# Optimization experiments

Measured on AMD Instinct MI355X. Metric: run time of the kernel, lower is better.

Reference implementation:

```python
import jax, jax.numpy as jnp
import numpy as np

C0, C1 = 16, 16
V, E = 100000, 1600000
TWO_PI = 6.2831853


def setup_inputs() -> dict:
    key = jax.random.key(0)
    ks = jax.random.split(key, 12)
    s0 = 1.0 / np.sqrt(C0)
    s1 = 1.0 / np.sqrt(C1)
    return {
        "x": jax.random.normal(ks[0], (V, C0 + 2 * C1), dtype=jnp.float32),
        "edge_index": jax.random.randint(ks[1], (2, E), 0, V, dtype=jnp.int64),
        "angles": jax.random.uniform(ks[2], (E,), dtype=jnp.float32) * TWO_PI,
        "transporters": jax.random.uniform(ks[3], (E,), dtype=jnp.float32) * TWO_PI,
        "e1": jax.random.normal(ks[4], (V, 3), dtype=jnp.float32),
        "e2": jax.random.normal(ks[5], (V, 3), dtype=jnp.float32),
        # mag head (out rho0): self rho0->rho0, neigh rho0->rho0 (const), neigh rho1->rho0 (2 basis coeffs/chan)
        "w_self0": jax.random.normal(ks[6], (C0,), dtype=jnp.float32) * s0,
        "w_n00": jax.random.normal(ks[7], (C0,), dtype=jnp.float32) * s0,
        "w_n10": jax.random.normal(ks[8], (C1, 2), dtype=jnp.float32) * s1,
        # tangent head (out rho1): self rho1->rho1 {I,J}, neigh rho0->rho1 (2), neigh rho1->rho1 (4)
        "w_self11": jax.random.normal(ks[9], (C1, 2), dtype=jnp.float32) * s1,
        "w_n01": jax.random.normal(ks[10], (C0, 2), dtype=jnp.float32) * s0,
        "w_n11": jax.random.normal(ks[11], (C1, 4), dtype=jnp.float32) * s1,
    }


def _gem_head(x, edge_index, angles, transporters,
              w_self0, w_n00, w_n10, w_self11, w_n01, w_n11):
    """Gauge-equivariant message passing (GEM-CNN style).
    Returns (tangent_coeffs (V,2), mag (V,))."""
    nV = x.shape[0]
    x0 = x[:, :C0]                       # (V, C0) scalar (rho0) channels
    x1 = x[:, C0:].reshape(nV, C1, 2)    # (V, C1, 2) vector (rho1) channels
    src, dst = edge_index[0], edge_index[1]

    # gather + parallel transport of rho1 features (rotate by transporter angle g)
    cg, sg = jnp.cos(transporters)[:, None], jnp.sin(transporters)[:, None]
    x1s = x1[src]                        # (E, C1, 2)
    u1 = cg * x1s[..., 0] - sg * x1s[..., 1]
    u2 = sg * x1s[..., 0] + cg * x1s[..., 1]
    x0s = x0[src]                        # (E, C0)

    ct, st = jnp.cos(angles)[:, None], jnp.sin(angles)[:, None]
    c2t, s2t = jnp.cos(2.0 * angles)[:, None], jnp.sin(2.0 * angles)[:, None]

    # ---- rho0 output (magnitude) messages ----
    # rho0->rho0: constant kernel; rho1->rho0: basis (cos,sin) and (-sin,cos)
    m0 = x0s @ w_n00 \
        + (ct * u1 + st * u2) @ w_n10[:, 0] \
        + (-st * u1 + ct * u2) @ w_n10[:, 1]          # (E,)

    # ---- rho1 output (tangent) messages ----
    # rho0->rho1: K = a*(cos,sin)^T + b*(-sin,cos)^T
    sa = x0s @ w_n01[:, 0]
    sb = x0s @ w_n01[:, 1]
    mv1 = sa * ct[:, 0] - sb * st[:, 0]
    mv2 = sa * st[:, 0] + sb * ct[:, 0]
    # rho1->rho1: basis {I, J, Refl(2t), J*Refl(2t)}
    p, q, r, s = w_n11[:, 0], w_n11[:, 1], w_n11[:, 2], w_n11[:, 3]
    r1 = c2t * u1 + s2t * u2
    r2 = s2t * u1 - c2t * u2
    mv1 = mv1 + u1 @ p - u2 @ q + r1 @ r - r2 @ s
    mv2 = mv2 + u2 @ p + u1 @ q + r2 @ r + r1 @ s

    # ---- mean aggregation over incoming edges ----
    deg = jax.ops.segment_sum(jnp.ones_like(m0), dst, num_segments=nV)
    denom = jnp.maximum(deg, 1.0)
    mag = jax.ops.segment_sum(m0, dst, num_segments=nV) / denom
    agg1 = jax.ops.segment_sum(mv1, dst, num_segments=nV) / denom
    agg2 = jax.ops.segment_sum(mv2, dst, num_segments=nV) / denom

    # ---- self kernels (Schur-allowed blocks only) ----
    mag = mag + x0 @ w_self0
    sa_, sb_ = w_self11[:, 0], w_self11[:, 1]
    t1 = agg1 + x1[..., 0] @ sa_ - x1[..., 1] @ sb_
    t2 = agg2 + x1[..., 1] @ sa_ + x1[..., 0] @ sb_
    return jnp.stack([t1, t2], axis=-1), mag


def reference(x, edge_index, angles, transporters, e1, e2,
              w_self0, w_n00, w_n10, w_self11, w_n01, w_n11):
    tangent, mag = _gem_head(x, edge_index, angles, transporters,
                             w_self0, w_n00, w_n10, w_self11, w_n01, w_n11)
    mag_scale = jax.nn.sigmoid(mag)[:, None] * 2.0      # (V,1)
    wss_3d = tangent[:, 0:1] * e1 + tangent[:, 1:2] * e2  # (V,3)
    return wss_3d * mag_scale
```

## Files before the change

kernel.cpp:

```cpp
#include <hip/hip_runtime.h>
#include <math.h>


#define VB 256
#define VB_SHIFT 8
#define MAXNB 400
#define CHUNK 3125
#define NCHUNK 512
#define BIGT 1024
#define FIXS 131072.0f
#define FIXSI (1.0f / 131072.0f)

typedef unsigned int uint32;

static __device__ __forceinline__ uint32 f2bf(float f) {
    uint32 u = __float_as_uint(f);
    return (u + 0x7FFFu + ((u >> 16) & 1u)) >> 16;
}
static __device__ __forceinline__ uint32 pack2(float lo, float hi) {
    return f2bf(lo) | (f2bf(hi) << 16);
}
static __device__ __forceinline__ float bf_lo(uint32 u) {
    return __uint_as_float(u << 16);
}
static __device__ __forceinline__ float bf_hi(uint32 u) {
    return __uint_as_float(u & 0xFFFF0000u);
}

__global__ __launch_bounds__(256)
void precompute_kernel(const float* __restrict__ x,
                       const float* __restrict__ w_self0,
                       const float* __restrict__ w_n00,
                       const float* __restrict__ w_n10,
                       const float* __restrict__ w_self11,
                       const float* __restrict__ w_n01,
                       const float* __restrict__ w_n11,
                       uint32* __restrict__ table,
                       float* __restrict__ selfbuf,
                       int V) {
    __shared__ float stage[256 * 49];
    int v0 = blockIdx.x * 256;
    int nv = min(256, V - v0);
    if (nv <= 0) return;
    int tid = threadIdx.x;
    {
        const float4* x4 = (const float4*)(x + (size_t)v0 * 48);
        int n4 = nv * 12;
        for (int j = tid; j < n4; j += 256) {
            float4 f = x4[j];
            float* dp = stage + (j / 12) * 49 + (j % 12) * 4;
            dp[0] = f.x; dp[1] = f.y; dp[2] = f.z; dp[3] = f.w;
        }
    }
    __syncthreads();
    if (tid >= nv) return;
    int v = v0 + tid;
    const float* xr = stage + tid * 49;
    float d00 = 0.f, aw0 = 0.f, bw0 = 0.f, aw1 = 0.f, bw1 = 0.f;
    float d01a = 0.f, d01b = 0.f;
    float aP = 0.f, bP = 0.f, aQ = 0.f, bQ = 0.f;
    float aR = 0.f, bR = 0.f, aS = 0.f, bS = 0.f;
    float selfmag = 0.f, t1s = 0.f, t2s = 0.f;
#pragma unroll
    for (int i = 0; i < 16; ++i) {
        float x0 = xr[i];
        float a  = xr[16 + 2 * i];
        float b  = xr[17 + 2 * i];
        d00     += x0 * w_n00[i];
        selfmag += x0 * w_self0[i];
        d01a    += x0 * w_n01[i * 2 + 0];
        d01b    += x0 * w_n01[i * 2 + 1];
        float w0 = w_n10[i * 2 + 0], w1 = w_n10[i * 2 + 1];
        aw0 += a * w0;  bw0 += b * w0;
        aw1 += a * w1;  bw1 += b * w1;
        float p = w_n11[i * 4 + 0], q = w_n11[i * 4 + 1];
        float r = w_n11[i * 4 + 2], s = w_n11[i * 4 + 3];
        aP += a * p;  bP += b * p;
        aQ += a * q;  bQ += b * q;
        aR += a * r;  bR += b * r;
        aS += a * s;  bS += b * s;
        float sa_ = w_self11[i * 2 + 0], sb_ = w_self11[i * 2 + 1];
        t1s += a * sa_ - b * sb_;
        t2s += b * sa_ + a * sb_;
    }
    uint4 w0, w1;
    w0.x = pack2(d00, aw0);  w0.y = pack2(bw0, aw1);
    w0.z = pack2(bw1, d01a); w0.w = pack2(d01b, aP);
    w1.x = pack2(bP, aQ);    w1.y = pack2(bQ, aR);
    w1.z = pack2(bR, aS);    w1.w = pack2(bS, 0.f);
    uint4* tp = (uint4*)(table + (size_t)v * 8);
    tp[0] = w0;  tp[1] = w1;
    float* sf = selfbuf + (size_t)v * 4;
    sf[0] = selfmag; sf[1] = t1s; sf[2] = t2s; sf[3] = 0.f;
}

__global__ __launch_bounds__(512)
void count_kernel(const int* __restrict__ dst,
                  int* __restrict__ cntmat,
                  int E, int NB) {
    __shared__ int hist[MAXNB];
    int b = blockIdx.x;
    int lo = b * CHUNK;
    int hi = min(E, lo + CHUNK);
    for (int i = threadIdx.x; i < NB; i += 512) hist[i] = 0;
    __syncthreads();
    for (int e = lo + threadIdx.x; e < hi; e += 512)
        atomicAdd(&hist[dst[e] >> VB_SHIFT], 1);
    __syncthreads();
    for (int i = threadIdx.x; i < NB; i += 512)
        cntmat[(size_t)i * NCHUNK + b] = hist[i];
}

__global__ __launch_bounds__(256)
void padscan_kernel(const int* __restrict__ cntmat,
                    int* __restrict__ padprefT,
                    int* __restrict__ padtotal,
                    int NB) {
    int lane = threadIdx.x & 63;
    int wv = threadIdx.x >> 6;
    int bin = blockIdx.x * 4 + wv;
    if (bin >= NB) return;
    const int* row = cntmat + (size_t)bin * NCHUNK;
    int c[8], p[8];
#pragma unroll
    for (int j = 0; j < 8; ++j) {
        c[j] = row[lane * 8 + j];
        p[j] = (c[j] + 7) & ~7;
    }
    int e[8];
    int run = 0;
#pragma unroll
    for (int j = 0; j < 8; ++j) { e[j] = run; run += p[j]; }
    int T = run;
    int incl = T;
#pragma unroll
    for (int d = 1; d < 64; d <<= 1) {
        int n = __shfl_up(incl, d);
        if (lane >= d) incl += n;
    }
    int base = incl - T;
#pragma unroll
    for (int j = 0; j < 8; ++j)
        padprefT[(size_t)(lane * 8 + j) * MAXNB + bin] = base + e[j];
    if (lane == 63) padtotal[bin] = incl;
}

__global__ __launch_bounds__(512)
void binbase_kernel(const int* __restrict__ padtotal,
                    int* __restrict__ binpadbase,
                    int NB) {
    __shared__ int wsum[8];
    int t = threadIdx.x;
    int lane = t & 63;
    int wv = t >> 6;
    int val = (t < NB) ? padtotal[t] : 0;
    int incl = val;
#pragma unroll
    for (int d = 1; d < 64; d <<= 1) {
        int n = __shfl_up(incl, d);
        if (lane >= d) incl += n;
    }
    if (lane == 63) wsum[wv] = incl;
    __syncthreads();
    if (t < 8) {
        int wval = wsum[t], winc = wval;
#pragma unroll
        for (int d = 1; d < 8; d <<= 1) {
            int n = __shfl_up(winc, d);
            if (lane >= d) winc += n;
        }
        wsum[t] = winc - wval;
    }
    __syncthreads();
    int ex = incl - val + wsum[wv];
    if (t < NB) binpadbase[t] = ex;
    if (t == NB - 1) binpadbase[NB] = ex + val;
}

__global__ __launch_bounds__(BIGT)
void scatter_kernel(const int* __restrict__ src,
                    const int* __restrict__ dst,
                    const float* __restrict__ angles,
                    const float* __restrict__ transporters,
                    const uint32* __restrict__ table,
                    const int* __restrict__ padprefT,
                    const int* __restrict__ binpadbase,
                    uint2* __restrict__ payload,
                    int E, int NB) {
    __shared__ int cnt_l[MAXNB];
    __shared__ int exoff_l[MAXNB];
    __shared__ int slot_l[MAXNB];
    __shared__ int wsum[16];
    __shared__ uint32 tw_src[CHUNK];
    __shared__ uint32 tw_ang[CHUNK];
    __shared__ uint32 tw_tr[CHUNK];
    __shared__ unsigned short tw_bin[CHUNK];

    int b = blockIdx.x;
    int lo = b * CHUNK;
    int hi = min(E, lo + CHUNK);
    int nloc = hi - lo;
    int tid = threadIdx.x;
    int lane = tid & 63;
    int wv = tid >> 6;

    for (int i = tid; i < NB; i += BIGT) cnt_l[i] = 0;
    __syncthreads();

    for (int e = lo + tid; e < hi; e += BIGT)
        atomicAdd(&cnt_l[dst[e] >> VB_SHIFT], 1);
    __syncthreads();

    int c = (tid < NB) ? cnt_l[tid] : 0;
    int incl = c;
#pragma unroll
    for (int d = 1; d < 64; d <<= 1) {
        int n = __shfl_up(incl, d);
        if (lane >= d) incl += n;
    }
    if (lane == 63) wsum[wv] = incl;
    __syncthreads();
    if (tid < 16) {
        int wval = wsum[tid], winc = wval;
#pragma unroll
        for (int d = 1; d < 16; d <<= 1) {
            int n = __shfl_up(winc, d);
            if (lane >= d) winc += n;
        }
        wsum[tid] = winc - wval;
    }
    __syncthreads();
    if (tid < NB) {
        int ex = incl - c + wsum[wv];
        exoff_l[tid] = ex;
        cnt_l[tid] = ex;
        slot_l[tid] = binpadbase[tid] + padprefT[(size_t)b * MAXNB + tid];
    }
    __syncthreads();

    for (int e = lo + tid; e < hi; e += BIGT) {
        int d = dst[e];
        int bin = d >> VB_SHIFT;
        uint32 dl = (uint32)(d & (VB - 1));
        int pos = atomicAdd(&cnt_l[bin], 1);
        tw_src[pos] = (uint32)src[e] | (dl << 17);
        tw_ang[pos] = __float_as_uint(angles[e]);
        tw_tr[pos]  = __float_as_uint(transporters[e]);
        tw_bin[pos] = (unsigned short)bin;
    }
    __syncthreads();

    for (int k = tid; k < nloc; k += BIGT) {
        int bin = (int)tw_bin[k];
        uint32 w0i = tw_src[k];
        int s  = (int)(w0i & 0x1FFFFu);
        int dl = (int)(w0i >> 17);
        float ang = __uint_as_float(tw_ang[k]);
        float trv = __uint_as_float(tw_tr[k]);
        float st, ct, sg, cg;
        sincosf(ang, &st, &ct);
        sincosf(trv, &sg, &cg);
        float c2t = ct * ct - st * st;
        float s2t = 2.0f * st * ct;

        const uint4* tp = (const uint4*)(table + (size_t)s * 8);
        uint4 W0 = tp[0], W1 = tp[1];
        float d00 = bf_lo(W0.x), aw0 = bf_hi(W0.x);
        float bw0 = bf_lo(W0.y), aw1 = bf_hi(W0.y);
        float bw1 = bf_lo(W0.z), d01a = bf_hi(W0.z);
        float d01b = bf_lo(W0.w), aP = bf_hi(W0.w);
        float bP = bf_lo(W1.x), aQ = bf_hi(W1.x);
        float bQ = bf_lo(W1.y), aR = bf_hi(W1.y);
        float bR = bf_lo(W1.z), aS = bf_hi(W1.z);
        float bS = bf_lo(W1.w);

        float u1w0 = cg * aw0 - sg * bw0, u2w0 = sg * aw0 + cg * bw0;
        float u1w1 = cg * aw1 - sg * bw1, u2w1 = sg * aw1 + cg * bw1;
        float m0 = d00 + ct * u1w0 + st * u2w0 - st * u1w1 + ct * u2w1;

        float u1p = cg * aP - sg * bP, u2p = sg * aP + cg * bP;
        float u1q = cg * aQ - sg * bQ, u2q = sg * aQ + cg * bQ;
        float u1r = cg * aR - sg * bR, u2r = sg * aR + cg * bR;
        float u1s = cg * aS - sg * bS, u2s = sg * aS + cg * bS;

        float mv1 = d01a * ct - d01b * st
                  + u1p - u2q
                  + c2t * u1r + s2t * u2r
                  - (s2t * u1s - c2t * u2s);
        float mv2 = d01a * st + d01b * ct
                  + u2p + u1q
                  + s2t * u1r - c2t * u2r
                  + c2t * u1s + s2t * u2s;

        uint2 pl;
        pl.x = pack2(m0, mv1);
        pl.y = f2bf(mv2) | ((uint32)dl << 16);
        payload[slot_l[bin] + (k - exoff_l[bin])] = pl;
    }
}

__global__ __launch_bounds__(BIGT)
void bucket_kernel(const uint2* __restrict__ payload,
                   const int* __restrict__ cntmat,
                   const int* __restrict__ padprefT,
                   const int* __restrict__ binpadbase,
                   const float* __restrict__ selfbuf,
                   const float* __restrict__ e1,
                   const float* __restrict__ e2,
                   float* __restrict__ out,
                   int V, int NB) {
    __shared__ int iacc[8][VB * 4];
    __shared__ int len_l[NCHUNK];
    __shared__ int pstart_l[NCHUNK];
    __shared__ unsigned short group2run[2048];
    int bin = blockIdx.x;
    int tid = threadIdx.x;
    for (int i = tid; i < 8 * VB * 4; i += BIGT) ((int*)iacc)[i] = 0;

    if (tid < NCHUNK) {
        int len = cntmat[(size_t)bin * NCHUNK + tid];
        int ps  = padprefT[(size_t)tid * MAXNB + bin];
        len_l[tid] = len;
        pstart_l[tid] = ps;
        int g0 = ps >> 3, gn = (len + 7) >> 3;
        for (int j = 0; j < gn; ++j)
            group2run[g0 + j] = (unsigned short)tid;
    }
    __syncthreads();

    int base = binpadbase[bin];
    int ptot = binpadbase[bin + 1] - base;
    int* myacc = iacc[tid >> 7];
    for (int k = tid; k < ptot; k += BIGT) {
        int r = (int)group2run[k >> 3];
        int local = k - pstart_l[r];
        if (local < len_l[r]) {
            uint2 pl = payload[base + k];
            float m0  = bf_lo(pl.x);
            float mv1 = bf_hi(pl.x);
            float mv2 = bf_lo(pl.y);
            int dl = (int)(pl.y >> 16);
            atomicAdd(&myacc[dl * 4 + 0], __float2int_rn(m0 * FIXS));
            atomicAdd(&myacc[dl * 4 + 1], __float2int_rn(mv1 * FIXS));
            atomicAdd(&myacc[dl * 4 + 2], __float2int_rn(mv2 * FIXS));
            atomicAdd(&myacc[dl * 4 + 3], 1);
        }
    }
    __syncthreads();
    if (tid < VB) {
        int v = bin * VB + tid;
        if (v < V) {
            int I0 = 0, I1 = 0, I2 = 0, I3 = 0;
#pragma unroll
            for (int w = 0; w < 8; ++w) {
                I0 += iacc[w][tid * 4 + 0];
                I1 += iacc[w][tid * 4 + 1];
                I2 += iacc[w][tid * 4 + 2];
                I3 += iacc[w][tid * 4 + 3];
            }
            float A0 = (float)I0 * FIXSI;
            float A1 = (float)I1 * FIXSI;
            float A2 = (float)I2 * FIXSI;
            float inv = 1.0f / fmaxf((float)I3, 1.0f);
            const float* sf = selfbuf + (size_t)v * 4;
            float mag = A0 * inv + sf[0];
            float t1  = A1 * inv + sf[1];
            float t2  = A2 * inv + sf[2];
            float scale = 2.0f / (1.0f + expf(-mag));
            float e1x = e1[v * 3 + 0], e1y = e1[v * 3 + 1], e1z = e1[v * 3 + 2];
            float e2x = e2[v * 3 + 0], e2y = e2[v * 3 + 1], e2z = e2[v * 3 + 2];
            out[v * 3 + 0] = (t1 * e1x + t2 * e2x) * scale;
            out[v * 3 + 1] = (t1 * e1y + t2 * e2y) * scale;
            out[v * 3 + 2] = (t1 * e1z + t2 * e2z) * scale;
        }
    }
}

extern "C" void kernel_launch(void* const* d_in, const int* in_sizes, int n_in,
                              void* d_out, int out_size, void* d_ws, size_t ws_size,
                              hipStream_t stream) {
    const float* x            = (const float*)d_in[0];
    const int*   edge_index   = (const int*)d_in[1];
    const float* angles       = (const float*)d_in[2];
    const float* transporters = (const float*)d_in[3];
    const float* e1           = (const float*)d_in[4];
    const float* e2           = (const float*)d_in[5];
    const float* w_self0      = (const float*)d_in[6];
    const float* w_n00        = (const float*)d_in[7];
    const float* w_n10        = (const float*)d_in[8];
    const float* w_self11     = (const float*)d_in[9];
    const float* w_n01        = (const float*)d_in[10];
    const float* w_n11        = (const float*)d_in[11];
    float* out = (float*)d_out;

    int V = in_sizes[0] / 48;
    int E = in_sizes[2];
    const int* src = edge_index;
    const int* dst = edge_index + E;

    int NB = (V + VB - 1) / VB;
    int nchunk = (E + CHUNK - 1) / CHUNK;

    char* p = (char*)d_ws;
    int* cntmat     = (int*)p;  p += (size_t)MAXNB * NCHUNK * 4;
    int* padprefT   = (int*)p;  p += (size_t)NCHUNK * MAXNB * 4;
    int* padtotal   = (int*)p;  p += (size_t)MAXNB * 4;
    int* binpadbase = (int*)p;  p += (size_t)(MAXNB + 1) * 4;
    uint32* table  = (uint32*)p;  p += (size_t)V * 8 * 4;
    float* selfbuf = (float*)p;   p += (size_t)V * 4 * 4;
    p = (char*)(((uintptr_t)p + 63) & ~(uintptr_t)63);
    uint2* payload = (uint2*)p;

    int gv = (V + 255) / 256;

    precompute_kernel<<<gv, 256, 0, stream>>>(x, w_self0, w_n00, w_n10,
                                              w_self11, w_n01, w_n11,
                                              table, selfbuf, V);
    count_kernel<<<nchunk, 512, 0, stream>>>(dst, cntmat, E, NB);
    padscan_kernel<<<(NB + 3) / 4, 256, 0, stream>>>(cntmat, padprefT,
                                                     padtotal, NB);
    binbase_kernel<<<1, 512, 0, stream>>>(padtotal, binpadbase, NB);
    scatter_kernel<<<nchunk, BIGT, 0, stream>>>(src, dst, angles,
                                                transporters, table,
                                                padprefT, binpadbase,
                                                payload, E, NB);
    bucket_kernel<<<NB, BIGT, 0, stream>>>(payload, cntmat, padprefT,
                                           binpadbase, selfbuf,
                                           e1, e2, out, V, NB);
}
```

Measured before the change: 141.9 us.

## Merge precompute and count kernels, pack LDS atomics into 64-bit, use fast sincos

The precompute and histogram-count kernels become one launch, with extra blocks doing the per-chunk destination histogram. This removes one kernel launch and lets the two independent phases overlap. The bucket kernel now packs four fixed-point accumulators into two 64-bit LDS atomics per edge instead of four 32-bit ones, using a bias so low-word carries cannot spill. The scatter kernel switches from sincosf to the __sinf/__cosf intrinsics, which are cheaper but less accurate.

```diff
diff --git a/kernel.cpp b/kernel.cpp
--- a/kernel.cpp
+++ b/kernel.cpp
@@ -10,8 +10,10 @@
 #define BIGT 1024
 #define FIXS 131072.0f
 #define FIXSI (1.0f / 131072.0f)
+#define BIASI (1 << 22)
 
 typedef unsigned int uint32;
+typedef unsigned long long uint64;
 
 static __device__ __forceinline__ uint32 f2bf(float f) {
     uint32 u = __float_as_uint(f);
@@ -28,21 +30,39 @@
 }
 
 __global__ __launch_bounds__(256)
-void precompute_kernel(const float* __restrict__ x,
-                       const float* __restrict__ w_self0,
-                       const float* __restrict__ w_n00,
-                       const float* __restrict__ w_n10,
-                       const float* __restrict__ w_self11,
-                       const float* __restrict__ w_n01,
-                       const float* __restrict__ w_n11,
-                       uint32* __restrict__ table,
-                       float* __restrict__ selfbuf,
-                       int V) {
+void precount_kernel(const float* __restrict__ x,
+                     const float* __restrict__ w_self0,
+                     const float* __restrict__ w_n00,
+                     const float* __restrict__ w_n10,
+                     const float* __restrict__ w_self11,
+                     const float* __restrict__ w_n01,
+                     const float* __restrict__ w_n11,
+                     uint32* __restrict__ table,
+                     float* __restrict__ selfbuf,
+                     const int* __restrict__ dst,
+                     int* __restrict__ cntmat,
+                     int V, int E, int GV, int NB) {
     __shared__ float stage[256 * 49];
+    int tid = threadIdx.x;
+
+    if ((int)blockIdx.x >= GV) {
+        int* hist = (int*)stage;
+        int b = blockIdx.x - GV;
+        int lo = b * CHUNK;
+        int hi = min(E, lo + CHUNK);
+        for (int i = tid; i < NB; i += 256) hist[i] = 0;
+        __syncthreads();
+        for (int e = lo + tid; e < hi; e += 256)
+            atomicAdd(&hist[dst[e] >> VB_SHIFT], 1);
+        __syncthreads();
+        for (int i = tid; i < NB; i += 256)
+            cntmat[(size_t)i * NCHUNK + b] = hist[i];
+        return;
+    }
+
     int v0 = blockIdx.x * 256;
     int nv = min(256, V - v0);
     if (nv <= 0) return;
-    int tid = threadIdx.x;
     {
         const float4* x4 = (const float4*)(x + (size_t)v0 * 48);
         int n4 = nv * 12;
@@ -94,23 +114,6 @@
     sf[0] = selfmag; sf[1] = t1s; sf[2] = t2s; sf[3] = 0.f;
 }
 
-__global__ __launch_bounds__(512)
-void count_kernel(const int* __restrict__ dst,
-                  int* __restrict__ cntmat,
-                  int E, int NB) {
-    __shared__ int hist[MAXNB];
-    int b = blockIdx.x;
-    int lo = b * CHUNK;
-    int hi = min(E, lo + CHUNK);
-    for (int i = threadIdx.x; i < NB; i += 512) hist[i] = 0;
-    __syncthreads();
-    for (int e = lo + threadIdx.x; e < hi; e += 512)
-        atomicAdd(&hist[dst[e] >> VB_SHIFT], 1);
-    __syncthreads();
-    for (int i = threadIdx.x; i < NB; i += 512)
-        cntmat[(size_t)i * NCHUNK + b] = hist[i];
-}
-
 __global__ __launch_bounds__(256)
 void padscan_kernel(const int* __restrict__ cntmat,
                     int* __restrict__ padprefT,
@@ -257,9 +260,8 @@
         int dl = (int)(w0i >> 17);
         float ang = __uint_as_float(tw_ang[k]);
         float trv = __uint_as_float(tw_tr[k]);
-        float st, ct, sg, cg;
-        sincosf(ang, &st, &ct);
-        sincosf(trv, &sg, &cg);
+        float st = __sinf(ang), ct = __cosf(ang);
+        float sg = __sinf(trv), cg = __cosf(trv);
         float c2t = ct * ct - st * st;
         float s2t = 2.0f * st * ct;
 
@@ -309,13 +311,13 @@
                    const float* __restrict__ e2,
                    float* __restrict__ out,
                    int V, int NB) {
-    __shared__ int iacc[8][VB * 4];
+    __shared__ uint64 acc[8][VB * 2];
     __shared__ int len_l[NCHUNK];
     __shared__ int pstart_l[NCHUNK];
     __shared__ unsigned short group2run[2048];
     int bin = blockIdx.x;
     int tid = threadIdx.x;
-    for (int i = tid; i < 8 * VB * 4; i += BIGT) ((int*)iacc)[i] = 0;
+    for (int i = tid; i < 8 * VB * 2; i += BIGT) ((uint64*)acc)[i] = 0ULL;
 
     if (tid < NCHUNK) {
         int len = cntmat[(size_t)bin * NCHUNK + tid];
@@ -330,7 +332,7 @@
 
     int base = binpadbase[bin];
     int ptot = binpadbase[bin + 1] - base;
-    int* myacc = iacc[tid >> 7];
+    uint64* myacc = acc[tid >> 7];
     for (int k = tid; k < ptot; k += BIGT) {
         int r = (int)group2run[k >> 3];
         int local = k - pstart_l[r];
@@ -340,28 +342,36 @@
             float mv1 = bf_hi(pl.x);
             float mv2 = bf_lo(pl.y);
             int dl = (int)(pl.y >> 16);
-            atomicAdd(&myacc[dl * 4 + 0], __float2int_rn(m0 * FIXS));
-            atomicAdd(&myacc[dl * 4 + 1], __float2int_rn(mv1 * FIXS));
-            atomicAdd(&myacc[dl * 4 + 2], __float2int_rn(mv2 * FIXS));
-            atomicAdd(&myacc[dl * 4 + 3], 1);
+            int m0f  = __float2int_rn(m0  * FIXS);
+            int mv1f = __float2int_rn(mv1 * FIXS);
+            int mv2f = __float2int_rn(mv2 * FIXS);
+            uint64 pa = (uint64)(uint32)(m0f + BIASI)
+                      | ((uint64)(uint32)mv1f << 32);
+            uint64 pb = (uint64)(uint32)(mv2f + BIASI)
+                      | (1ULL << 32);
+            atomicAdd(&myacc[dl * 2 + 0], pa);
+            atomicAdd(&myacc[dl * 2 + 1], pb);
         }
     }
     __syncthreads();
     if (tid < VB) {
         int v = bin * VB + tid;
         if (v < V) {
-            int I0 = 0, I1 = 0, I2 = 0, I3 = 0;
+            int cnt = 0, m0s = 0, mv1s = 0, mv2s = 0;
 #pragma unroll
             for (int w = 0; w < 8; ++w) {
-                I0 += iacc[w][tid * 4 + 0];
-                I1 += iacc[w][tid * 4 + 1];
-                I2 += iacc[w][tid * 4 + 2];
-                I3 += iacc[w][tid * 4 + 3];
+                uint64 a = acc[w][tid * 2 + 0];
+                uint64 b = acc[w][tid * 2 + 1];
+                uint32 nw = (uint32)(b >> 32);
+                cnt  += (int)nw;
+                m0s  += (int)((uint32)a - nw * (uint32)BIASI);
+                mv1s += (int)(a >> 32);
+                mv2s += (int)((uint32)b - nw * (uint32)BIASI);
             }
-            float A0 = (float)I0 * FIXSI;
-            float A1 = (float)I1 * FIXSI;
-            float A2 = (float)I2 * FIXSI;
-            float inv = 1.0f / fmaxf((float)I3, 1.0f);
+            float A0 = (float)m0s  * FIXSI;
+            float A1 = (float)mv1s * FIXSI;
+            float A2 = (float)mv2s * FIXSI;
+            float inv = 1.0f / fmaxf((float)cnt, 1.0f);
             const float* sf = selfbuf + (size_t)v * 4;
             float mag = A0 * inv + sf[0];
             float t1  = A1 * inv + sf[1];
@@ -413,10 +423,9 @@
 
     int gv = (V + 255) / 256;
 
-    precompute_kernel<<<gv, 256, 0, stream>>>(x, w_self0, w_n00, w_n10,
-                                              w_self11, w_n01, w_n11,
-                                              table, selfbuf, V);
-    count_kernel<<<nchunk, 512, 0, stream>>>(dst, cntmat, E, NB);
+    precount_kernel<<<gv + nchunk, 256, 0, stream>>>(
+        x, w_self0, w_n00, w_n10, w_self11, w_n01, w_n11,
+        table, selfbuf, dst, cntmat, V, E, gv, NB);
     padscan_kernel<<<(NB + 3) / 4, 256, 0, stream>>>(cntmat, padprefT,
                                                      padtotal, NB);
     binbase_kernel<<<1, 512, 0, stream>>>(padtotal, binpadbase, NB);
```

After: 144.1 us. About the same (+1.5%).
